# Kernel tuning notes

Hardware: AMD Instinct MI355X
Metric: run time of the kernel (lower is better)

Reference implementation:

```python
import jax, jax.numpy as jnp
import numpy as np

N = 8192
F_IN = 256
F_OUT = 128
ALPHA = 0.2  # leaky relu slope
NEG_INF = -9e15


def setup_inputs() -> dict:
    key = jax.random.key(0)
    k_x, k_w, k_a, k_adj = jax.random.split(key, 4)
    x = jax.random.normal(k_x, (N, F_IN), dtype=jnp.float32)
    # xavier_uniform for W
    limit = np.sqrt(6.0 / (F_IN + F_OUT)).astype(np.float32)
    W = jax.random.uniform(k_w, (F_IN, F_OUT), minval=-limit, maxval=limit, dtype=jnp.float32)
    a = jax.random.normal(k_a, (2 * F_OUT, 1), dtype=jnp.float32) * 0.1
    adj = (jax.random.uniform(k_adj, (N, N)) < 0.01).astype(jnp.float32)
    adj = jnp.maximum(adj, jnp.eye(N, dtype=jnp.float32))
    return {"x": x, "adj": adj, "W": W, "a": a}


def reference(x, adj, W, a):
    # h = X W : [N, F_OUT]
    h = x @ W
    # e_ij = leakyrelu([h_i || h_j] . a) = leakyrelu((h a1)_i + (h a2)_j)
    a1 = a[:F_OUT, 0]  # [F_OUT]
    a2 = a[F_OUT:, 0]  # [F_OUT]
    e = (h @ a1)[:, None] + (h @ a2)[None, :]  # [N, N]
    e = jnp.where(e > 0, e, ALPHA * e)  # LeakyReLU
    att = jnp.where(adj > 0.0, e, NEG_INF)
    att = jax.nn.softmax(att, axis=1)  # row softmax over neighbors
    # dropout p=0.0 -> identity
    h_prime = att @ h  # [N, F_OUT]
    # concat=True -> ELU
    return jax.nn.elu(h_prime)
```

## Files before the change

kernel.cpp:

```cpp
#include <hip/hip_runtime.h>
#include <math.h>

#define N 8192
#define F_IN 256
#define F_OUT 128
#define ALPHA 0.2f
#define CAP 256

__global__ __launch_bounds__(256) void gemm_xw(const float* __restrict__ x,
                                               const float* __restrict__ W,
                                               float* __restrict__ h) {
    __shared__ float xs[32][64];
    __shared__ float ws[64][128];
    const int row0 = blockIdx.x * 32;
    const int t = threadIdx.x;
    const int rg = t >> 5;
    const int cg = t & 31;
    float acc[4][4] = {};

    for (int k0 = 0; k0 < F_IN; k0 += 64) {
        #pragma unroll
        for (int i = 0; i < 2; ++i) {
            int fi = t + i * 256;
            int r  = fi >> 4;
            int c4 = fi & 15;
            float4 v = *(const float4*)(&x[(size_t)(row0 + r) * F_IN + k0 + c4 * 4]);
            *(float4*)(&xs[r][c4 * 4]) = v;
        }
        #pragma unroll
        for (int i = 0; i < 8; ++i) {
            int fi = t + i * 256;
            int r  = fi >> 5;
            int c4 = fi & 31;
            float4 v = *(const float4*)(&W[(size_t)(k0 + r) * F_OUT + c4 * 4]);
            *(float4*)(&ws[r][c4 * 4]) = v;
        }
        __syncthreads();
        #pragma unroll 8
        for (int kk = 0; kk < 64; ++kk) {
            float4 wv = *(const float4*)(&ws[kk][cg * 4]);
            #pragma unroll
            for (int r = 0; r < 4; ++r) {
                float xv = xs[rg * 4 + r][kk];
                acc[r][0] += xv * wv.x;
                acc[r][1] += xv * wv.y;
                acc[r][2] += xv * wv.z;
                acc[r][3] += xv * wv.w;
            }
        }
        __syncthreads();
    }
    #pragma unroll
    for (int r = 0; r < 4; ++r) {
        float4 v = make_float4(acc[r][0], acc[r][1], acc[r][2], acc[r][3]);
        *(float4*)(&h[(size_t)(row0 + rg * 4 + r) * F_OUT + cg * 4]) = v;
    }
}

__global__ __launch_bounds__(256) void compute_s(const float* __restrict__ h,
                                                 const float* __restrict__ a,
                                                 float* __restrict__ s1,
                                                 float* __restrict__ s2) {
    __shared__ float r1[4], r2[4];
    const int t = threadIdx.x;
    const int row = blockIdx.x * 2 + (t >> 7);
    const int f = t & 127;
    float hv = h[(size_t)row * F_OUT + f];
    float v1 = hv * a[f];
    float v2 = hv * a[F_OUT + f];
    #pragma unroll
    for (int o = 32; o > 0; o >>= 1) {
        v1 += __shfl_down(v1, o);
        v2 += __shfl_down(v2, o);
    }
    if ((t & 63) == 0) { r1[t >> 6] = v1; r2[t >> 6] = v2; }
    __syncthreads();
    if ((t & 127) == 0) {
        int w = t >> 6;
        s1[row] = r1[w] + r1[w + 1];
        s2[row] = r2[w] + r2[w + 1];
    }
}

__global__ __launch_bounds__(256) void scan_adj(const float* __restrict__ adj,
                                                unsigned short* __restrict__ idx,
                                                int* __restrict__ cnt) {
    const int wave = threadIdx.x >> 6;
    const int lane = threadIdx.x & 63;
    const int row = blockIdx.x * 4 + wave;
    const float4* __restrict__ arow = (const float4*)(adj + (size_t)row * N);
    unsigned short* __restrict__ outp = idx + (size_t)row * CAP;
    const unsigned long long lt = (lane == 63) ? 0x7fffffffffffffffULL
                                               : ((1ULL << lane) - 1ULL);
    int c = 0;
    for (int it = 0; it < 32; it += 4) {
        float4 vv[4];
        vv[0] = arow[(it + 0) * 64 + lane];
        vv[1] = arow[(it + 1) * 64 + lane];
        vv[2] = arow[(it + 2) * 64 + lane];
        vv[3] = arow[(it + 3) * 64 + lane];
        #pragma unroll
        for (int q = 0; q < 4; ++q) {
            const int base = ((it + q) * 64 + lane) * 4;
            float vals[4] = {vv[q].x, vv[q].y, vv[q].z, vv[q].w};
            #pragma unroll
            for (int u = 0; u < 4; ++u) {
                unsigned long long m = __ballot(vals[u] > 0.0f);
                if (vals[u] > 0.0f) {
                    int pos = c + __popcll(m & lt);
                    if (pos < CAP) outp[pos] = (unsigned short)(base + u);
                }
                c += (int)__popcll(m);
            }
        }
    }
    if (lane == 0) cnt[row] = c;
}

__global__ __launch_bounds__(256) void attn_gather(const unsigned short* __restrict__ idx,
                                                   const int* __restrict__ cnt,
                                                   const float* __restrict__ h,
                                                   const float* __restrict__ s1,
                                                   const float* __restrict__ s2,
                                                   float* __restrict__ out) {
    __shared__ float wv[CAP];
    __shared__ unsigned short js[CAP];
    __shared__ float red1[4], red2[4];
    __shared__ float part[128];

    const int i = blockIdx.x;
    const int t = threadIdx.x;
    const int lane = t & 63;
    const int wave = t >> 6;
    const int K = min(cnt[i], CAP);

    float e = -INFINITY;
    int j = 0;
    if (t < K) {
        j = idx[(size_t)i * CAP + t];
        float v = s1[i] + s2[j];
        e = v > 0.0f ? v : ALPHA * v;
    }
    float m = e;
    #pragma unroll
    for (int o = 32; o > 0; o >>= 1) m = fmaxf(m, __shfl_xor(m, o));
    if (lane == 0) red1[wave] = m;
    __syncthreads();
    m = fmaxf(fmaxf(red1[0], red1[1]), fmaxf(red1[2], red1[3]));

    float w = (t < K) ? expf(e - m) : 0.0f;
    float s = w;
    #pragma unroll
    for (int o = 32; o > 0; o >>= 1) s += __shfl_xor(s, o);
    if (lane == 0) red2[wave] = s;
    wv[t] = w;
    js[t] = (unsigned short)j;
    __syncthreads();
    const float invl = 1.0f / (red2[0] + red2[1] + red2[2] + red2[3]);

    const int g = t >> 7;
    const int f = t & 127;
    float acc = 0.0f;
    int k = g;
    for (; k + 6 < K; k += 8) {
        float w0 = wv[k],     w1 = wv[k + 2], w2 = wv[k + 4], w3 = wv[k + 6];
        int   j0 = js[k],     j1 = js[k + 2], j2 = js[k + 4], j3 = js[k + 6];
        float h0 = h[(size_t)j0 * F_OUT + f];
        float h1 = h[(size_t)j1 * F_OUT + f];
        float h2 = h[(size_t)j2 * F_OUT + f];
        float h3 = h[(size_t)j3 * F_OUT + f];
        acc += w0 * h0 + w1 * h1 + w2 * h2 + w3 * h3;
    }
    for (; k < K; k += 2) acc += wv[k] * h[(size_t)js[k] * F_OUT + f];

    if (g == 1) part[f] = acc;
    __syncthreads();
    if (g == 0) {
        float v = (acc + part[f]) * invl;
        v = v > 0.0f ? v : expm1f(v);
        out[(size_t)i * F_OUT + f] = v;
    }
}

extern "C" void kernel_launch(void* const* d_in, const int* in_sizes, int n_in,
                              void* d_out, int out_size, void* d_ws, size_t ws_size,
                              hipStream_t stream) {
    const float* x   = (const float*)d_in[0];
    const float* adj = (const float*)d_in[1];
    const float* W   = (const float*)d_in[2];
    const float* a   = (const float*)d_in[3];
    float* out = (float*)d_out;

    float* h  = (float*)d_ws;
    float* s1 = h + (size_t)N * F_OUT;
    float* s2 = s1 + N;
    int*   cnt = (int*)(s2 + N);
    unsigned short* idx = (unsigned short*)(cnt + N);

    gemm_xw<<<N / 32, 256, 0, stream>>>(x, W, h);
    compute_s<<<N / 2, 256, 0, stream>>>(h, a, s1, s2);
    scan_adj<<<N / 4, 256, 0, stream>>>(adj, idx, cnt);
    attn_gather<<<N, 256, 0, stream>>>(idx, cnt, h, s1, s2, out);
}
```

Baseline: 412.9 us.

## Fuse GEMM, score projection and adjacency scan into one heterogeneous launch

```diff
diff --git a/kernel.cpp b/kernel.cpp
--- a/kernel.cpp
+++ b/kernel.cpp
@@ -6,115 +6,104 @@
 #define F_OUT 128
 #define ALPHA 0.2f
 #define CAP 256
+#define GEMM_BLOCKS 256
 
-__global__ __launch_bounds__(256) void gemm_xw(const float* __restrict__ x,
-                                               const float* __restrict__ W,
-                                               float* __restrict__ h) {
-    __shared__ float xs[32][64];
-    __shared__ float ws[64][128];
-    const int row0 = blockIdx.x * 32;
+__global__ __launch_bounds__(256) void fused_gemm_scan(const float* __restrict__ x,
+                                                       const float* __restrict__ W,
+                                                       const float* __restrict__ a,
+                                                       const float* __restrict__ adj,
+                                                       float* __restrict__ h,
+                                                       float* __restrict__ s1,
+                                                       float* __restrict__ s2,
+                                                       unsigned short* __restrict__ idx,
+                                                       int* __restrict__ cnt) {
+    __shared__ float xst[64][36];
+
     const int t = threadIdx.x;
-    const int rg = t >> 5;
-    const int cg = t & 31;
-    float acc[4][4] = {};
+    if (blockIdx.x < GEMM_BLOCKS) {
+        const int row0 = blockIdx.x * 32;
+        const int rg = t >> 5;
+        const int cg = t & 31;
+        float acc[4][4] = {};
 
-    for (int k0 = 0; k0 < F_IN; k0 += 64) {
-        #pragma unroll
-        for (int i = 0; i < 2; ++i) {
-            int fi = t + i * 256;
-            int r  = fi >> 4;
-            int c4 = fi & 15;
-            float4 v = *(const float4*)(&x[(size_t)(row0 + r) * F_IN + k0 + c4 * 4]);
-            *(float4*)(&xs[r][c4 * 4]) = v;
+        for (int k0 = 0; k0 < F_IN; k0 += 64) {
+            #pragma unroll
+            for (int i = 0; i < 2; ++i) {
+                int fi = t + i * 256;
+                int r  = fi >> 4;
+                int c4 = fi & 15;
+                float4 v = *(const float4*)(&x[(size_t)(row0 + r) * F_IN + k0 + c4 * 4]);
+                xst[c4 * 4 + 0][r] = v.x;
+                xst[c4 * 4 + 1][r] = v.y;
+                xst[c4 * 4 + 2][r] = v.z;
+                xst[c4 * 4 + 3][r] = v.w;
+            }
+            __syncthreads();
+            #pragma unroll 8
+            for (int kk = 0; kk < 64; ++kk) {
+                float4 wv = *(const float4*)(&W[(size_t)(k0 + kk) * F_OUT + cg * 4]);
+                float4 xv = *(const float4*)(&xst[kk][rg * 4]);
+                acc[0][0] += xv.x * wv.x; acc[0][1] += xv.x * wv.y;
+                acc[0][2] += xv.x * wv.z; acc[0][3] += xv.x * wv.w;
+                acc[1][0] += xv.y * wv.x; acc[1][1] += xv.y * wv.y;
+                acc[1][2] += xv.y * wv.z; acc[1][3] += xv.y * wv.w;
+                acc[2][0] += xv.z * wv.x; acc[2][1] += xv.z * wv.y;
+                acc[2][2] += xv.z * wv.z; acc[2][3] += xv.z * wv.w;
+                acc[3][0] += xv.w * wv.x; acc[3][1] += xv.w * wv.y;
+                acc[3][2] += xv.w * wv.z; acc[3][3] += xv.w * wv.w;
+            }
+            __syncthreads();
         }
         #pragma unroll
-        for (int i = 0; i < 8; ++i) {
-            int fi = t + i * 256;
-            int r  = fi >> 5;
-            int c4 = fi & 31;
-            float4 v = *(const float4*)(&W[(size_t)(k0 + r) * F_OUT + c4 * 4]);
-            *(float4*)(&ws[r][c4 * 4]) = v;
+        for (int r = 0; r < 4; ++r) {
+            float4 v = make_float4(acc[r][0], acc[r][1], acc[r][2], acc[r][3]);
+            *(float4*)(&h[(size_t)(row0 + rg * 4 + r) * F_OUT + cg * 4]) = v;
         }
-        __syncthreads();
-        #pragma unroll 8
-        for (int kk = 0; kk < 64; ++kk) {
-            float4 wv = *(const float4*)(&ws[kk][cg * 4]);
+        float4 a1 = *(const float4*)(&a[cg * 4]);
+        float4 a2 = *(const float4*)(&a[F_OUT + cg * 4]);
+        #pragma unroll
+        for (int r = 0; r < 4; ++r) {
+            float v1 = acc[r][0] * a1.x + acc[r][1] * a1.y + acc[r][2] * a1.z + acc[r][3] * a1.w;
+            float v2 = acc[r][0] * a2.x + acc[r][1] * a2.y + acc[r][2] * a2.z + acc[r][3] * a2.w;
             #pragma unroll
-            for (int r = 0; r < 4; ++r) {
-                float xv = xs[rg * 4 + r][kk];
-                acc[r][0] += xv * wv.x;
-                acc[r][1] += xv * wv.y;
-                acc[r][2] += xv * wv.z;
-                acc[r][3] += xv * wv.w;
+            for (int o = 16; o > 0; o >>= 1) {
+                v1 += __shfl_xor(v1, o);
+                v2 += __shfl_xor(v2, o);
+            }
+            if (((t & 63) & 31) == 0) {
+                s1[row0 + rg * 4 + r] = v1;
+                s2[row0 + rg * 4 + r] = v2;
             }
         }
-        __syncthreads();
-    }
-    #pragma unroll
-    for (int r = 0; r < 4; ++r) {
-        float4 v = make_float4(acc[r][0], acc[r][1], acc[r][2], acc[r][3]);
-        *(float4*)(&h[(size_t)(row0 + rg * 4 + r) * F_OUT + cg * 4]) = v;
-    }
-}
-
-__global__ __launch_bounds__(256) void compute_s(const float* __restrict__ h,
-                                                 const float* __restrict__ a,
-                                                 float* __restrict__ s1,
-                                                 float* __restrict__ s2) {
-    __shared__ float r1[4], r2[4];
-    const int t = threadIdx.x;
-    const int row = blockIdx.x * 2 + (t >> 7);
-    const int f = t & 127;
-    float hv = h[(size_t)row * F_OUT + f];
-    float v1 = hv * a[f];
-    float v2 = hv * a[F_OUT + f];
-    #pragma unroll
-    for (int o = 32; o > 0; o >>= 1) {
-        v1 += __shfl_down(v1, o);
-        v2 += __shfl_down(v2, o);
-    }
-    if ((t & 63) == 0) { r1[t >> 6] = v1; r2[t >> 6] = v2; }
-    __syncthreads();
-    if ((t & 127) == 0) {
-        int w = t >> 6;
-        s1[row] = r1[w] + r1[w + 1];
-        s2[row] = r2[w] + r2[w + 1];
-    }
-}
-
-__global__ __launch_bounds__(256) void scan_adj(const float* __restrict__ adj,
-                                                unsigned short* __restrict__ idx,
-                                                int* __restrict__ cnt) {
-    const int wave = threadIdx.x >> 6;
-    const int lane = threadIdx.x & 63;
-    const int row = blockIdx.x * 4 + wave;
-    const float4* __restrict__ arow = (const float4*)(adj + (size_t)row * N);
-    unsigned short* __restrict__ outp = idx + (size_t)row * CAP;
-    const unsigned long long lt = (lane == 63) ? 0x7fffffffffffffffULL
-                                               : ((1ULL << lane) - 1ULL);
-    int c = 0;
-    for (int it = 0; it < 32; it += 4) {
-        float4 vv[4];
-        vv[0] = arow[(it + 0) * 64 + lane];
-        vv[1] = arow[(it + 1) * 64 + lane];
-        vv[2] = arow[(it + 2) * 64 + lane];
-        vv[3] = arow[(it + 3) * 64 + lane];
-        #pragma unroll
-        for (int q = 0; q < 4; ++q) {
-            const int base = ((it + q) * 64 + lane) * 4;
-            float vals[4] = {vv[q].x, vv[q].y, vv[q].z, vv[q].w};
+    } else {
+        const int wave = t >> 6;
+        const int lane = t & 63;
+        const int row = (blockIdx.x - GEMM_BLOCKS) * 4 + wave;
+        const float4* __restrict__ arow = (const float4*)(adj + (size_t)row * N);
+        unsigned short* __restrict__ outp = idx + (size_t)row * CAP;
+        const unsigned long long lt = (1ULL << lane) - 1ULL;
+        int c = 0;
+        for (int it = 0; it < 32; it += 8) {
+            float4 vv[8];
             #pragma unroll
-            for (int u = 0; u < 4; ++u) {
-                unsigned long long m = __ballot(vals[u] > 0.0f);
-                if (vals[u] > 0.0f) {
-                    int pos = c + __popcll(m & lt);
-                    if (pos < CAP) outp[pos] = (unsigned short)(base + u);
+            for (int q = 0; q < 8; ++q) vv[q] = arow[(it + q) * 64 + lane];
+            #pragma unroll
+            for (int q = 0; q < 8; ++q) {
+                const int base = ((it + q) * 64 + lane) * 4;
+                float vals[4] = {vv[q].x, vv[q].y, vv[q].z, vv[q].w};
+                #pragma unroll
+                for (int u = 0; u < 4; ++u) {
+                    unsigned long long m = __ballot(vals[u] > 0.0f);
+                    if (vals[u] > 0.0f) {
+                        int pos = c + __popcll(m & lt);
+                        if (pos < CAP) outp[pos] = (unsigned short)(base + u);
+                    }
+                    c += (int)__popcll(m);
                 }
-                c += (int)__popcll(m);
             }
         }
+        if (lane == 0) cnt[row] = c;
     }
-    if (lane == 0) cnt[row] = c;
 }
 
 __global__ __launch_bounds__(256) void attn_gather(const unsigned short* __restrict__ idx,
@@ -197,8 +186,6 @@
     int*   cnt = (int*)(s2 + N);
     unsigned short* idx = (unsigned short*)(cnt + N);
 
-    gemm_xw<<<N / 32, 256, 0, stream>>>(x, W, h);
-    compute_s<<<N / 2, 256, 0, stream>>>(h, a, s1, s2);
-    scan_adj<<<N / 4, 256, 0, stream>>>(adj, idx, cnt);
+    fused_gemm_scan<<<GEMM_BLOCKS + N / 4, 256, 0, stream>>>(x, W, a, adj, h, s1, s2, idx, cnt);
     attn_gather<<<N, 256, 0, stream>>>(idx, cnt, h, s1, s2, out);
 }
```

Result: faster. 395.7 us (-4.2%).
